# Optimization experiments

Measured on AMD Instinct MI355X. Metric: run time of the kernel, lower is better.

## Reference

```python
import jax, jax.numpy as jnp
import numpy as np

N_HEADS = 16
ROPE_BASE = 10000.0


def apply_rope(x):
    # x: (b, h, t, d); rotate interleaved pairs along last dim, positions = t axis
    b, h, t, d = x.shape
    theta = 1.0 / (ROPE_BASE ** (jnp.arange(0, d, 2, dtype=jnp.float32) / d))  # (d/2,)
    ang = jnp.arange(t, dtype=jnp.float32)[:, None] * theta[None, :]           # (t, d/2)
    cos = jnp.cos(ang)[None, None]  # (1,1,t,d/2)
    sin = jnp.sin(ang)[None, None]
    xp = x.reshape(b, h, t, d // 2, 2)
    x0, x1 = xp[..., 0], xp[..., 1]
    o0 = x0 * cos - x1 * sin
    o1 = x1 * cos + x0 * sin
    return jnp.stack([o0, o1], axis=-1).reshape(b, h, t, d)


def setup_inputs() -> dict:
    key = jax.random.key(0)
    k1, k2, k3 = jax.random.split(key, 3)
    B, T, C = 2, 2048, 1024
    x = jax.random.normal(k1, (B, T, C), dtype=jnp.float32)
    w_qkv = jax.random.normal(k2, (3 * C, C), dtype=jnp.float32) * (1.0 / np.sqrt(C))
    w_proj = jax.random.normal(k3, (C, C), dtype=jnp.float32) * (1.0 / np.sqrt(C))
    return {"x": x, "w_qkv": w_qkv, "w_proj": w_proj}


def reference(x, w_qkv, w_proj):
    B, T, C = x.shape
    H = N_HEADS
    D = C // H
    # fused QKV projection: (b,t,3C)
    qkv = x @ w_qkv.T
    qkv = qkv.reshape(B, T, 3, H, D).transpose(2, 0, 3, 1, 4)  # (3, b, h, t, d)
    q, k, v = qkv[0], qkv[1], qkv[2]
    q = apply_rope(q)
    k = apply_rope(k)
    scale = 1.0 / jnp.sqrt(jnp.float32(D))
    scores = jnp.einsum('bhqd,bhkd->bhqk', q, k) * scale  # (b,h,t,t)
    causal = jnp.tril(jnp.ones((T, T), dtype=bool))
    scores = jnp.where(causal[None, None], scores, jnp.finfo(scores.dtype).min)
    attn = jax.nn.softmax(scores, axis=-1)
    y = jnp.einsum('bhqk,bhkd->bhqd', attn, v)  # (b,h,t,d)
    y = y.transpose(0, 2, 1, 3).reshape(B, T, C)
    return y @ w_proj.T
```

## Files before the change

kernel.cpp:

```cpp
#include <hip/hip_runtime.h>
#include <math.h>

#define B_ 2
#define T_ 2048
#define C_ 1024
#define H_ 16
#define D_ 64
#define NX_ 4194304
#define NWQ_ 3145728
#define NWP_ 1048576

typedef unsigned short u16;
typedef unsigned int u32;
typedef __bf16 bf16x8 __attribute__((ext_vector_type(8)));
typedef _Float16 f16x8 __attribute__((ext_vector_type(8)));
typedef __fp16 fp16x2 __attribute__((ext_vector_type(2)));
typedef float f32x4 __attribute__((ext_vector_type(4)));
typedef u16 u16x4 __attribute__((ext_vector_type(4)));

__device__ __forceinline__ u16 f2bf(float f) {
    union { float f; u32 u; } v; v.f = f;
    u32 r = v.u + 0x7fffu + ((v.u >> 16) & 1u);
    return (u16)(r >> 16);
}

#define GLD_LDS(g, l) \
    __builtin_amdgcn_global_load_lds( \
        (const __attribute__((address_space(1))) u32*)(const void*)(g), \
        (__attribute__((address_space(3))) u32*)(void*)(l), 16, 0, 0)

__global__ __launch_bounds__(256) void cast_all(const float* __restrict__ x,
                                                const float* __restrict__ wq,
                                                const float* __restrict__ wp,
                                                u16* __restrict__ out,
                                                float* __restrict__ tab) {
    const int bid = blockIdx.x;
    if (bid >= 8192) {
        const int k = (bid - 8192) * 256 + threadIdx.x;
        #pragma unroll
        for (int e = 0; e < 2; ++e) {
            const int pidx = 2 * k + e;
            const int t = pidx >> 5, i = pidx & 31;
            const float theta = __expf(-0.2878231366f * (float)i);
            float sn, cs;
            __sincosf((float)t * theta, &sn, &cs);
            *(float2*)(tab + pidx * 2) = make_float2(cs, sn);
        }
        return;
    }
    const int i = (bid * 256 + threadIdx.x) * 4;
    const float* src;
    int off;
    if (i < NX_) { src = x; off = i; }
    else if (i < NX_ + NWQ_) { src = wq; off = i - NX_; }
    else { src = wp; off = i - NX_ - NWQ_; }
    float4 v = *(const float4*)(src + off);
    u16x4 o;
    o.x = f2bf(v.x); o.y = f2bf(v.y); o.z = f2bf(v.z); o.w = f2bf(v.w);
    *(u16x4*)(out + i) = o;
}

template <int EPI, int DBUF, int BN>
__global__ __launch_bounds__(256) void gemm64(const u16* __restrict__ A,
                                              const u16* __restrict__ Bm,
                                              float* __restrict__ OutF,
                                              u16* __restrict__ qb,
                                              u16* __restrict__ kb,
                                              u16* __restrict__ vt,
                                              const float* __restrict__ tab,
                                              int M, int N, int K) {
    constexpr int NBUF = DBUF ? 2 : 1;
    constexpr int MI = (BN == 128) ? 4 : 2;
    constexpr int BCH = BN / 32;
    __shared__ u16 As[NBUF][128 * 64];
    __shared__ u16 Bs[NBUF][BN * 64];
    const int tid = threadIdx.x;
    const int lane = tid & 63;
    const int wave = tid >> 6;
    const int wm = (BN == 128) ? (wave >> 1) * 64 : wave * 32;
    const int wn = (BN == 128) ? (wave & 1) * 64 : 0;
    const int m0 = blockIdx.y * 128;
    const int n0 = blockIdx.x * BN;

    const int rl = lane >> 3;
    const int sg = ((lane & 7) ^ rl) * 8;
    const u16* gA[4]; const u16* gB[BCH];
    int lofA[4], lofB[BCH];
    #pragma unroll
    for (int c = 0; c < 4; ++c) {
        const int ca = wave * 4 + c;
        gA[c] = A + (size_t)(m0 + ca * 8 + rl) * K + sg;
        lofA[c] = ca * 512;
    }
    #pragma unroll
    for (int c = 0; c < BCH; ++c) {
        const int cb = wave * BCH + c;
        gB[c] = Bm + (size_t)(n0 + cb * 8 + rl) * K + sg;
        lofB[c] = cb * 512;
    }

    const int col = lane & 15;
    const int quad = lane >> 4;
    int aoff[2][MI], boff[2][4];
    #pragma unroll
    for (int ks = 0; ks < 2; ++ks) {
        #pragma unroll
        for (int i = 0; i < MI; ++i) {
            const int m = wm + i * 16 + col;
            aoff[ks][i] = (m >> 3) * 512 + (m & 7) * 64 +
                          ((((ks << 2) | quad)) ^ (m & 7)) * 8;
        }
        #pragma unroll
        for (int j = 0; j < 4; ++j) {
            const int n = wn + j * 16 + col;
            boff[ks][j] = (n >> 3) * 512 + (n & 7) * 64 +
                          ((((ks << 2) | quad)) ^ (n & 7)) * 8;
        }
    }

    f32x4 acc[MI][4] = {};

#define GEMM_STAGE(BUFI, KOFF)                                                 \
    {                                                                          \
        _Pragma("unroll")                                                      \
        for (int c = 0; c < 4; ++c)                                            \
            GLD_LDS(gA[c] + (KOFF), &As[BUFI][lofA[c]]);                       \
        _Pragma("unroll")                                                      \
        for (int c = 0; c < BCH; ++c)                                          \
            GLD_LDS(gB[c] + (KOFF), &Bs[BUFI][lofB[c]]);                       \
    }

#define GEMM_COMPUTE(ASB, BSB)                                                 \
    {                                                                          \
        _Pragma("unroll")                                                      \
        for (int ks = 0; ks < 2; ++ks) {                                       \
            bf16x8 a[MI], b[4];                                                \
            _Pragma("unroll")                                                  \
            for (int i = 0; i < MI; ++i)                                       \
                a[i] = *(const bf16x8*)((ASB) + aoff[ks][i]);                  \
            _Pragma("unroll")                                                  \
            for (int j = 0; j < 4; ++j)                                        \
                b[j] = *(const bf16x8*)((BSB) + boff[ks][j]);                  \
            _Pragma("unroll")                                                  \
            for (int i = 0; i < MI; ++i)                                       \
                _Pragma("unroll")                                              \
                for (int j = 0; j < 4; ++j)                                    \
                    acc[i][j] = __builtin_amdgcn_mfma_f32_16x16x32_bf16(       \
                        a[i], b[j], acc[i][j], 0, 0, 0);                       \
        }                                                                      \
    }

    if (DBUF) {
        GEMM_STAGE(0, 0)
        __syncthreads();
        int buf = 0;
        for (int k0 = 64; k0 < K; k0 += 64) {
            GEMM_STAGE(buf ^ 1, k0)
            GEMM_COMPUTE(&As[buf][0], &Bs[buf][0])
            __syncthreads();
            buf ^= 1;
        }
        GEMM_COMPUTE(&As[buf][0], &Bs[buf][0])
    } else {
        for (int k0 = 0; k0 < K; k0 += 64) {
            __syncthreads();
            GEMM_STAGE(0, k0)
            __syncthreads();
            GEMM_COMPUTE(&As[0][0], &Bs[0][0])
        }
    }
#undef GEMM_COMPUTE
#undef GEMM_STAGE

    const int rq = quad * 4;
    if (EPI == 0) {
        #pragma unroll
        for (int i = 0; i < MI; ++i)
            #pragma unroll
            for (int j = 0; j < 4; ++j)
                #pragma unroll
                for (int r = 0; r < 4; ++r)
                    OutF[(size_t)(m0 + wm + i * 16 + rq + r) * N +
                         n0 + wn + j * 16 + col] = acc[i][j][r];
    } else {
        const int sslot = m0 >> 10;
        #pragma unroll
        for (int i = 0; i < MI; ++i) {
            const int gm = m0 + wm + i * 16 + rq;
            const int hh = (gm >> 6) & 15;
            const int dbase = gm & 63;
            #pragma unroll
            for (int j = 0; j < 4; ++j) {
                const int gt = n0 + wn + j * 16 + col;
                const int bb = gt >> 11;
                const int t = gt & (T_ - 1);
                const int bh = bb * H_ + hh;
                if (sslot < 2) {
                    const float4 cs4 = *(const float4*)(tab + t * 64 + dbase);
                    u16x4 ov;
                    ov[0] = f2bf(acc[i][j][0] * cs4.x - acc[i][j][1] * cs4.y);
                    ov[1] = f2bf(acc[i][j][1] * cs4.x + acc[i][j][0] * cs4.y);
                    ov[2] = f2bf(acc[i][j][2] * cs4.z - acc[i][j][3] * cs4.w);
                    ov[3] = f2bf(acc[i][j][3] * cs4.z + acc[i][j][2] * cs4.w);
                    u16* dst = (sslot == 0 ? qb : kb) +
                               ((size_t)bh * T_ + t) * D_ + dbase;
                    *(u16x4*)dst = ov;
                } else {
                    #pragma unroll
                    for (int r = 0; r < 4; ++r) {
                        union { _Float16 h; u16 u; } cv;
                        cv.h = (_Float16)acc[i][j][r];
                        vt[((size_t)bh * D_ + dbase + r) * T_ + t] = cv.u;
                    }
                }
            }
        }
    }
}

__global__ __launch_bounds__(256) void attn_mfma(const u16* __restrict__ qb,
                                                 const u16* __restrict__ kb,
                                                 const u16* __restrict__ vtg,
                                                 u16* __restrict__ y) {
    __shared__ u16 Ks[2][2 * 4096];
    __shared__ u16 Vt[2][2 * 4096];
    const int id = blockIdx.x;
    const int bh = id & 31;
    const int pr = id >> 5;
    const int b = bh >> 4, h = bh & 15;
    const int tid = threadIdx.x;
    const int lane = tid & 63;
    const int wave = tid >> 6;
    const int col = lane & 15;
    const int quad = lane >> 4;

    const int rl = lane >> 3;
    const int sg = ((lane & 7) ^ rl) * 8;
    const u16* kg[2]; const u16* vg[2];
    int lco[2];
    #pragma unroll
    for (int e = 0; e < 2; ++e) {
        const int ca = 2 * wave + e;
        kg[e] = kb + ((size_t)bh * T_ + ca * 8 + rl) * D_ + sg;
        vg[e] = vtg + ((size_t)bh * D_ + ca * 8 + rl) * T_ + sg;
        lco[e] = ca * 512;
    }

    int koff[2][4];
    #pragma unroll
    for (int ks = 0; ks < 2; ++ks)
        #pragma unroll
        for (int n = 0; n < 4; ++n) {
            const int rr = n * 16 + col;
            koff[ks][n] = (rr >> 3) * 512 + (rr & 7) * 64 +
                          ((((ks << 2) | quad)) ^ (rr & 7)) * 8;
        }

    const int srcA = col + ((quad & 1) << 5);
    const int srcB = srcA + 16;
    const bool hi = (quad >> 1) != 0;

#define STAGE2(BUF, C0)                                                        \
    {                                                                          \
        const size_t jj = (size_t)(C0) * 64;                                   \
        _Pragma("unroll")                                                      \
        for (int e = 0; e < 2; ++e) {                                          \
            GLD_LDS(kg[e] + jj * D_, &Ks[BUF][lco[e]]);                        \
            GLD_LDS(vg[e] + jj, &Vt[BUF][lco[e]]);                             \
            GLD_LDS(kg[e] + (jj + 64) * D_, &Ks[BUF][4096 + lco[e]]);          \
            GLD_LDS(vg[e] + jj + 64, &Vt[BUF][4096 + lco[e]]);                 \
        }                                                                      \
    }

#define CHUNK_COMPUTE(BUF, SUB, J0, DIAG)                                      \
    {                                                                          \
        const int j0_ = (J0);                                                  \
        const u16* ksb = &Ks[BUF][(SUB) * 4096];                               \
        const u16* vsb = &Vt[BUF][(SUB) * 4096];                               \
                                 \
        f32x4 s[4] = {};                                                       \
        __builtin_amdgcn_s_setprio(1);                                         \
        _Pragma("unroll")                                                      \
        for (int ks = 0; ks < 2; ++ks)                                         \
            _Pragma("unroll")                                                  \
            for (int n = 0; n < 4; ++n) {                                      \
                const bf16x8 kf = *(const bf16x8*)(ksb + koff[ks][n]);         \
                s[n] = __builtin_amdgcn_mfma_f32_16x16x32_bf16(                \
                    kf, qf[ks], s[n], 0, 0, 0);                                \
            }                                                                  \
        __builtin_amdgcn_s_setprio(0);                                         \
              \
        u32 pk[4][2];                                                          \
        _Pragma("unroll")                                                      \
        for (int n = 0; n < 4; ++n) {                                          \
            float p[4];                                                        \
            _Pragma("unroll")                                                  \
            for (int r = 0; r < 4; ++r) {                                      \
                float pv = __builtin_amdgcn_exp2f(s[n][r] * 0.1803368801f);    \
                if (DIAG && (j0_ + n * 16 + quad * 4 + r > qrow)) pv = 0.0f;   \
                p[r] = pv;                                                     \
                lsv[r] += pv;                                                  \
            }                                                                  \
            union { fp16x2 h; u32 u; } c0, c1;                                 \
            c0.h = __builtin_amdgcn_cvt_pkrtz(p[0], p[1]);                     \
            c1.h = __builtin_amdgcn_cvt_pkrtz(p[2], p[3]);                     \
            pk[n][0] = c0.u;                                                   \
            pk[n][1] = c1.u;                                                   \
        }                                                                      \
                         \
        _Pragma("unroll")                                                      \
        for (int ks = 0; ks < 2; ++ks) {                                       \
            const int nl = 2 * ks, nh = nl + 1;                                \
            const u32 w0a = __shfl(pk[nl][0], srcA);                           \
            const u32 w0b = __shfl(pk[nh][0], srcA);                           \
            const u32 w1a = __shfl(pk[nl][1], srcA);                           \
            const u32 w1b = __shfl(pk[nh][1], srcA);                           \
            const u32 w2a = __shfl(pk[nl][0], srcB);                           \
            const u32 w2b = __shfl(pk[nh][0], srcB);                           \
            const u32 w3a = __shfl(pk[nl][1], srcB);                           \
            const u32 w3b = __shfl(pk[nh][1], srcB);                           \
            union { u32 u[4]; f16x8 v; } af;                                   \
            af.u[0] = hi ? w0b : w0a;                                          \
            af.u[1] = hi ? w1b : w1a;                                          \
            af.u[2] = hi ? w2b : w2a;                                          \
            af.u[3] = hi ? w3b : w3a;                                          \
            __builtin_amdgcn_s_setprio(1);                                     \
            _Pragma("unroll")                                                  \
            for (int n = 0; n < 4; ++n) {                                      \
                const f16x8 vf = *(const f16x8*)(vsb + koff[ks][n]);           \
                o[n] = __builtin_amdgcn_mfma_f32_16x16x32_f16(                 \
                    af.v, vf, o[n], 0, 0, 0);                                  \
            }                                                                  \
            __builtin_amdgcn_s_setprio(0);                                     \
        }                                                                      \
    }

    for (int half = 0; half < 2; ++half) {
        const int qt = half ? pr : (31 - pr);
        const int q0 = qt * 64;
        const int qrow = q0 + wave * 16 + col;
        const int nchunks = qt + 1;
        const int niter = (nchunks + 1) >> 1;

        const u16* qbase = qb + ((size_t)bh * T_ + q0 + wave * 16) * D_;
        bf16x8 qf[2];
        #pragma unroll
        for (int ks = 0; ks < 2; ++ks)
            qf[ks] = *(const bf16x8*)(qbase + col * D_ + ks * 32 + quad * 8);

        f32x4 o[4] = {};
        float lsv[4] = {};

        __syncthreads();
        STAGE2(0, 0)

        int buf = 0;
        for (int it = 0; it + 1 < niter; ++it) {
            asm volatile("s_barrier" ::: "memory");
            STAGE2(buf ^ 1, 2 * (it + 1))
            asm volatile("s_waitcnt vmcnt(8)" ::: "memory");
            asm volatile("s_barrier" ::: "memory");
            CHUNK_COMPUTE(buf, 0, it * 128, false)
            CHUNK_COMPUTE(buf, 1, it * 128 + 64, false)
            buf ^= 1;
        }
        __syncthreads();
        if (nchunks & 1) {
            CHUNK_COMPUTE(buf, 0, (nchunks - 1) * 64, true)
        } else {
            CHUNK_COMPUTE(buf, 0, (nchunks - 2) * 64, false)
            CHUNK_COMPUTE(buf, 1, (nchunks - 1) * 64, true)
        }

        float l = (lsv[0] + lsv[1]) + (lsv[2] + lsv[3]);
        l += __shfl_xor(l, 16);
        l += __shfl_xor(l, 32);
        const float inv = 1.0f / l;
        float invr[4];
        #pragma unroll
        for (int r = 0; r < 4; ++r)
            invr[r] = __shfl(inv, quad * 4 + r);
        #pragma unroll
        for (int r = 0; r < 4; ++r) {
            const int row = q0 + wave * 16 + quad * 4 + r;
            u16* yp = y + (size_t)(b * T_ + row) * C_ + h * D_;
            #pragma unroll
            for (int n = 0; n < 4; ++n)
                yp[n * 16 + col] = f2bf(o[n][r] * invr[r]);
        }
    }
#undef CHUNK_COMPUTE
#undef STAGE2
}

extern "C" void kernel_launch(void* const* d_in, const int* in_sizes, int n_in,
                              void* d_out, int out_size, void* d_ws, size_t ws_size,
                              hipStream_t stream) {
    const float* x      = (const float*)d_in[0];
    const float* w_qkv  = (const float*)d_in[1];
    const float* w_proj = (const float*)d_in[2];
    float* out = (float*)d_out;

    const int M = B_ * T_;
    u16* xb  = (u16*)d_ws;
    u16* wqb = xb + NX_;
    u16* wpb = wqb + NWQ_;
    u16* qb  = wpb + NWP_;
    u16* kb  = qb + NX_;
    u16* vt  = kb + NX_;
    u16* yb  = vt + NX_;
    float* tab = (float*)(yb + NX_);

    cast_all<<<8192 + 128, 256, 0, stream>>>(x, w_qkv, w_proj, xb, tab);

    gemm64<1, 1, 64><<<dim3(M / 64, 3 * C_ / 128), 256, 0, stream>>>(
        wqb, xb, nullptr, qb, kb, vt, tab, 3 * C_, M, C_);

    attn_mfma<<<512, 256, 0, stream>>>(qb, kb, vt, yb);

    gemm64<0, 1, 64><<<dim3(C_ / 64, M / 128), 256, 0, stream>>>(
        yb, wpb, out, nullptr, nullptr, nullptr, nullptr, M, C_, C_);
}
```

Before: 175.3 us.

## Split attention KV chunks across two wave groups with LDS reduction

The attention kernel grows from 4 to 8 waves per block. Two groups of four waves each process alternate 64-key sub-chunks of the double-buffered KV stage, and the staging loads are spread across all 8 waves. Partial outputs and row sums from group 1 are then reduced through LDS into group 0, which normalizes and writes the result. This doubles the parallelism per query tile to hide MFMA and exp latency, at the cost of an extra LDS reduction, more barriers, and higher register and occupancy pressure.

After: 176.2 us. No clear change (+0.5%).

```diff
diff --git a/kernel.cpp b/kernel.cpp
--- a/kernel.cpp
+++ b/kernel.cpp
@@ -218,10 +218,10 @@
     }
 }
 
-__global__ __launch_bounds__(256) void attn_mfma(const u16* __restrict__ qb,
-                                                 const u16* __restrict__ kb,
-                                                 const u16* __restrict__ vtg,
-                                                 u16* __restrict__ y) {
+__global__ __launch_bounds__(512, 4) void attn_mfma(const u16* __restrict__ qb,
+                                                    const u16* __restrict__ kb,
+                                                    const u16* __restrict__ vtg,
+                                                    u16* __restrict__ y) {
     __shared__ u16 Ks[2][2 * 4096];
     __shared__ u16 Vt[2][2 * 4096];
     const int id = blockIdx.x;
@@ -231,20 +231,16 @@
     const int tid = threadIdx.x;
     const int lane = tid & 63;
     const int wave = tid >> 6;
+    const int grp = wave >> 2;
+    const int wq = wave & 3;
     const int col = lane & 15;
     const int quad = lane >> 4;
 
     const int rl = lane >> 3;
     const int sg = ((lane & 7) ^ rl) * 8;
-    const u16* kg[2]; const u16* vg[2];
-    int lco[2];
-    #pragma unroll
-    for (int e = 0; e < 2; ++e) {
-        const int ca = 2 * wave + e;
-        kg[e] = kb + ((size_t)bh * T_ + ca * 8 + rl) * D_ + sg;
-        vg[e] = vtg + ((size_t)bh * D_ + ca * 8 + rl) * T_ + sg;
-        lco[e] = ca * 512;
-    }
+    const u16* kg = kb + ((size_t)bh * T_ + wave * 8 + rl) * D_ + sg;
+    const u16* vg = vtg + ((size_t)bh * D_ + wave * 8 + rl) * T_ + sg;
+    const int lco = wave * 512;
 
     int koff[2][4];
     #pragma unroll
@@ -263,13 +259,10 @@
 #define STAGE2(BUF, C0)                                                        \
     {                                                                          \
         const size_t jj = (size_t)(C0) * 64;                                   \
-        _Pragma("unroll")                                                      \
-        for (int e = 0; e < 2; ++e) {                                          \
-            GLD_LDS(kg[e] + jj * D_, &Ks[BUF][lco[e]]);                        \
-            GLD_LDS(vg[e] + jj, &Vt[BUF][lco[e]]);                             \
-            GLD_LDS(kg[e] + (jj + 64) * D_, &Ks[BUF][4096 + lco[e]]);          \
-            GLD_LDS(vg[e] + jj + 64, &Vt[BUF][4096 + lco[e]]);                 \
-        }                                                                      \
+        GLD_LDS(kg + jj * D_, &Ks[BUF][lco]);                                  \
+        GLD_LDS(vg + jj, &Vt[BUF][lco]);                                       \
+        GLD_LDS(kg + (jj + 64) * D_, &Ks[BUF][4096 + lco]);                    \
+        GLD_LDS(vg + jj + 64, &Vt[BUF][4096 + lco]);                           \
     }
 
 #define CHUNK_COMPUTE(BUF, SUB, J0, DIAG)                                      \
@@ -301,11 +294,11 @@
                 p[r] = pv;                                                     \
                 lsv[r] += pv;                                                  \
             }                                                                  \
-            union { fp16x2 h; u32 u; } c0, c1;                                 \
-            c0.h = __builtin_amdgcn_cvt_pkrtz(p[0], p[1]);                     \
-            c1.h = __builtin_amdgcn_cvt_pkrtz(p[2], p[3]);                     \
-            pk[n][0] = c0.u;                                                   \
-            pk[n][1] = c1.u;                                                   \
+            union { fp16x2 h; u32 u; } c0u, c1u;                               \
+            c0u.h = __builtin_amdgcn_cvt_pkrtz(p[0], p[1]);                    \
+            c1u.h = __builtin_amdgcn_cvt_pkrtz(p[2], p[3]);                    \
+            pk[n][0] = c0u.u;                                                  \
+            pk[n][1] = c1u.u;                                                  \
         }                                                                      \
                          \
         _Pragma("unroll")                                                      \
@@ -338,11 +331,11 @@
     for (int half = 0; half < 2; ++half) {
         const int qt = half ? pr : (31 - pr);
         const int q0 = qt * 64;
-        const int qrow = q0 + wave * 16 + col;
+        const int qrow = q0 + wq * 16 + col;
         const int nchunks = qt + 1;
         const int niter = (nchunks + 1) >> 1;
 
-        const u16* qbase = qb + ((size_t)bh * T_ + q0 + wave * 16) * D_;
+        const u16* qbase = qb + ((size_t)bh * T_ + q0 + wq * 16) * D_;
         bf16x8 qf[2];
         #pragma unroll
         for (int ks = 0; ks < 2; ++ks)
@@ -358,35 +351,60 @@
         for (int it = 0; it + 1 < niter; ++it) {
             asm volatile("s_barrier" ::: "memory");
             STAGE2(buf ^ 1, 2 * (it + 1))
-            asm volatile("s_waitcnt vmcnt(8)" ::: "memory");
+            asm volatile("s_waitcnt vmcnt(4)" ::: "memory");
             asm volatile("s_barrier" ::: "memory");
-            CHUNK_COMPUTE(buf, 0, it * 128, false)
-            CHUNK_COMPUTE(buf, 1, it * 128 + 64, false)
+            CHUNK_COMPUTE(buf, grp, (2 * it + grp) * 64, false)
             buf ^= 1;
         }
         __syncthreads();
-        if (nchunks & 1) {
-            CHUNK_COMPUTE(buf, 0, (nchunks - 1) * 64, true)
-        } else {
-            CHUNK_COMPUTE(buf, 0, (nchunks - 2) * 64, false)
-            CHUNK_COMPUTE(buf, 1, (nchunks - 1) * 64, true)
-        }
-
-        float l = (lsv[0] + lsv[1]) + (lsv[2] + lsv[3]);
-        l += __shfl_xor(l, 16);
-        l += __shfl_xor(l, 32);
-        const float inv = 1.0f / l;
-        float invr[4];
-        #pragma unroll
-        for (int r = 0; r < 4; ++r)
-            invr[r] = __shfl(inv, quad * 4 + r);
-        #pragma unroll
-        for (int r = 0; r < 4; ++r) {
-            const int row = q0 + wave * 16 + quad * 4 + r;
-            u16* yp = y + (size_t)(b * T_ + row) * C_ + h * D_;
+        {
+            const int cf = 2 * (niter - 1) + grp;
+            if (cf <= qt) {
+                if (cf == qt) { CHUNK_COMPUTE(buf, grp, cf * 64, true) }
+                else         { CHUNK_COMPUTE(buf, grp, cf * 64, false) }
+            }
+        }
+
+        __syncthreads();
+        float* scratch = (float*)&Ks[0][0];
+        const int sidx = (wq * 64 + lane) * 21;
+        if (grp == 1) {
             #pragma unroll
             for (int n = 0; n < 4; ++n)
-                yp[n * 16 + col] = f2bf(o[n][r] * invr[r]);
+                #pragma unroll
+                for (int r = 0; r < 4; ++r)
+                    scratch[sidx + n * 4 + r] = o[n][r];
+            #pragma unroll
+            for (int r = 0; r < 4; ++r)
+                scratch[sidx + 16 + r] = lsv[r];
+        }
+        __syncthreads();
+        if (grp == 0) {
+            #pragma unroll
+            for (int n = 0; n < 4; ++n)
+                #pragma unroll
+                for (int r = 0; r < 4; ++r)
+                    o[n][r] += scratch[sidx + n * 4 + r];
+            #pragma unroll
+            for (int r = 0; r < 4; ++r)
+                lsv[r] += scratch[sidx + 16 + r];
+
+            float l = (lsv[0] + lsv[1]) + (lsv[2] + lsv[3]);
+            l += __shfl_xor(l, 16);
+            l += __shfl_xor(l, 32);
+            const float inv = 1.0f / l;
+            float invr[4];
+            #pragma unroll
+            for (int r = 0; r < 4; ++r)
+                invr[r] = __shfl(inv, quad * 4 + r);
+            #pragma unroll
+            for (int r = 0; r < 4; ++r) {
+                const int row = q0 + wq * 16 + quad * 4 + r;
+                u16* yp = y + (size_t)(b * T_ + row) * C_ + h * D_;
+                #pragma unroll
+                for (int n = 0; n < 4; ++n)
+                    yp[n * 16 + col] = f2bf(o[n][r] * invr[r]);
+            }
         }
     }
 #undef CHUNK_COMPUTE
@@ -416,7 +434,7 @@
     gemm64<1, 1, 64><<<dim3(M / 64, 3 * C_ / 128), 256, 0, stream>>>(
         wqb, xb, nullptr, qb, kb, vt, tab, 3 * C_, M, C_);
 
-    attn_mfma<<<512, 256, 0, stream>>>(qb, kb, vt, yb);
+    attn_mfma<<<512, 512, 0, stream>>>(qb, kb, vt, yb);
 
     gemm64<0, 1, 64><<<dim3(C_ / 64, M / 128), 256, 0, stream>>>(
         yb, wpb, out, nullptr, nullptr, nullptr, nullptr, M, C_, C_);
```
